# Performance work log

Measured on AMD Instinct MI355X. Metric: run time of the kernel, lower is better.

## Reference

```python
import jax, jax.numpy as jnp
import numpy as np

N, E, B = 30000, 60000, 500          # nodes, edges, graphs
NODE_IN, EDGE_IN, H, R = 64, 16, 64, 1024
MP_STEPS, S2S_STEPS = 3, 3           # num_step_message_passing, num_step_set2set
D = 2 * H                            # Set2Set in_channels / LSTM hidden size


def setup_inputs() -> dict:
    key = jax.random.key(0)
    ks = jax.random.split(key, 20)
    g = lambda i, shape, s: jax.random.normal(ks[i], shape, jnp.float32) * s
    return {
        "x": g(0, (N, NODE_IN), 1.0),
        "edge_index": jax.random.randint(ks[1], (2, E), 0, N),
        "edge_attr": g(2, (E, EDGE_IN), 1.0),
        "batch": jnp.sort(jax.random.randint(ks[3], (N,), 0, B)),
        # project_node_feats
        "W_proj": g(4, (NODE_IN, H), 0.1), "b_proj": jnp.zeros((H,), jnp.float32),
        # NNConv edge network + root + bias
        "W_edge": g(5, (EDGE_IN, H * H), 0.05), "b_edge": jnp.zeros((H * H,), jnp.float32),
        "root": g(6, (H, H), 0.1), "conv_bias": jnp.zeros((H,), jnp.float32),
        # GRU (torch gate order r, z, n)
        "gru_W_ih": g(7, (3 * H, H), 0.1), "gru_W_hh": g(8, (3 * H, H), 0.1),
        "gru_b_ih": jnp.zeros((3 * H,), jnp.float32), "gru_b_hh": jnp.zeros((3 * H,), jnp.float32),
        # node classifier head
        "W_cls": g(9, (H, 1), 0.1), "b_cls": jnp.zeros((1,), jnp.float32),
        # Set2Set LSTM: input 2D (=4H), hidden D (=2H), gate order i, f, g, o
        "lstm_W_ih": g(10, (4 * D, 2 * D), 0.1), "lstm_W_hh": g(11, (4 * D, D), 0.1),
        "lstm_b_ih": jnp.zeros((4 * D,), jnp.float32), "lstm_b_hh": jnp.zeros((4 * D,), jnp.float32),
        # sparsify (Linear 4H->R + PReLU)
        "W_sp": g(12, (4 * H, R), 0.05), "b_sp": jnp.zeros((R,), jnp.float32),
        "prelu_a": jnp.float32(0.25),
        "W_y1": g(13, (R, 128), 0.05), "b_y1": jnp.zeros((128,), jnp.float32),
        "W_y2": g(14, (128, 1), 0.1), "b_y2": jnp.zeros((1,), jnp.float32),
    }


def reference(x, edge_index, edge_attr, batch,
              W_proj, b_proj, W_edge, b_edge, root, conv_bias,
              gru_W_ih, gru_W_hh, gru_b_ih, gru_b_hh,
              W_cls, b_cls,
              lstm_W_ih, lstm_W_hh, lstm_b_ih, lstm_b_hh,
              W_sp, b_sp, prelu_a, W_y1, b_y1, W_y2, b_y2):
    src, dst = edge_index[0], edge_index[1]
    h0 = jax.nn.relu(x @ W_proj + b_proj)                  # [N, H]
    # Per-edge HxH weight matrices (loop-invariant; NNConv recomputes same values).
    We = (edge_attr @ W_edge + b_edge).reshape(E, H, H)    # [E, H, H]

    node, hidden = h0, h0
    for _ in range(MP_STEPS):
        msg = jnp.einsum('eh,eho->eo', node[src], We)      # gather + per-edge matvec
        aggr = jax.ops.segment_sum(msg, dst, num_segments=N)
        m = jax.nn.relu(aggr + node @ root + conv_bias)    # NNConv output + activation
        # GRU cell (seq_len=1)
        gi = m @ gru_W_ih.T + gru_b_ih
        gh = hidden @ gru_W_hh.T + gru_b_hh
        r = jax.nn.sigmoid(gi[:, :H] + gh[:, :H])
        z = jax.nn.sigmoid(gi[:, H:2 * H] + gh[:, H:2 * H])
        n = jnp.tanh(gi[:, 2 * H:] + r * gh[:, 2 * H:])
        hidden = (1.0 - z) * n + z * hidden
        node = hidden

    xcat = jnp.concatenate([h0, node], axis=1)             # [N, 2H] = [N, D]
    p_borylation = (node @ W_cls + b_cls)[:, 0]            # [N]

    # Set2Set over xcat
    q_star = jnp.zeros((B, 2 * D), xcat.dtype)
    hs = jnp.zeros((B, D), xcat.dtype)
    cs = jnp.zeros((B, D), xcat.dtype)
    for _ in range(S2S_STEPS):
        gts = q_star @ lstm_W_ih.T + lstm_b_ih + hs @ lstm_W_hh.T + lstm_b_hh
        i_g = jax.nn.sigmoid(gts[:, :D])
        f_g = jax.nn.sigmoid(gts[:, D:2 * D])
        g_g = jnp.tanh(gts[:, 2 * D:3 * D])
        o_g = jax.nn.sigmoid(gts[:, 3 * D:])
        cs = f_g * cs + i_g * g_g
        hs = o_g * jnp.tanh(cs)
        q = hs                                             # [B, D]
        e = jnp.sum(xcat * q[batch], axis=-1)              # [N]
        mseg = jax.ops.segment_max(e, batch, num_segments=B)
        ex = jnp.exp(e - mseg[batch])
        denom = jax.ops.segment_sum(ex, batch, num_segments=B)
        a = ex / denom[batch]                              # segment softmax
        rvec = jax.ops.segment_sum(a[:, None] * xcat, batch, num_segments=B)
        q_star = jnp.concatenate([q, rvec], axis=1)        # [B, 2D] = [B, 4H]

    gf = q_star @ W_sp + b_sp
    gf = jnp.where(gf >= 0, gf, prelu_a * gf)              # PReLU
    predicted_yield = (jax.nn.relu(gf @ W_y1 + b_y1) @ W_y2 + b_y2)[:, 0]
    return p_borylation, predicted_yield
```

## Files before the change

kernel.cpp:

```cpp
#include <hip/hip_runtime.h>
#include <math.h>

#define NN 30000
#define NNP 30080
#define NE 60000
#define NB 500
#define YGH 256
#define KE 1088

typedef __attribute__((ext_vector_type(8))) short bf16x8;
typedef __attribute__((ext_vector_type(4))) float f32x4;

__device__ __forceinline__ float sigmoidf_(float x) { return 1.0f / (1.0f + expf(-x)); }

__device__ __forceinline__ unsigned short bf_hi(float x) {
  unsigned int u = __float_as_uint(x);
  u += 0x7FFF + ((u >> 16) & 1);
  return (unsigned short)(u >> 16);
}
__device__ __forceinline__ float bf_f(unsigned short h) {
  return __uint_as_float(((unsigned int)h) << 16);
}
__device__ __forceinline__ void split_bf(float x, unsigned short& hi, unsigned short& lo) {
  hi = bf_hi(x);
  lo = bf_hi(x - bf_f(hi));
}

__device__ __forceinline__ int lower_bound_i(const int* __restrict__ a, int n, int v) {
  int lo = 0, hi = n;
  while (lo < hi) { int mid = (lo + hi) >> 1; if (a[mid] < v) lo = mid + 1; else hi = mid; }
  return lo;
}

__global__ __launch_bounds__(256) void gemm_mfma_k(
    const unsigned short* __restrict__ Ahi, const unsigned short* __restrict__ Alo,
    const unsigned short* __restrict__ Bhi, const unsigned short* __restrict__ Blo,
    float* __restrict__ C, int ldc,
    float* __restrict__ C2,
    unsigned short* __restrict__ Chi, unsigned short* __restrict__ Clo,
    const float* __restrict__ bias, int M, int flags)
{
  const int tid = threadIdx.x;
  const int wid = tid >> 6, lane = tid & 63;
  const int l15 = lane & 15, l4 = lane >> 4;
  const int r0 = blockIdx.x * 128 + (wid >> 1) * 64;
  const int c0 = blockIdx.y * 64 + (wid & 1) * 32;

  f32x4 acc[4][2];
#pragma unroll
  for (int rt = 0; rt < 4; rt++)
#pragma unroll
    for (int ct = 0; ct < 2; ct++) acc[rt][ct] = (f32x4){0.f, 0.f, 0.f, 0.f};

#pragma unroll
  for (int ks = 0; ks < 2; ks++) {
    const int kb = ks * 32 + l4 * 8;
    bf16x8 a_h[4], a_l[4], b_h[2], b_l[2];
#pragma unroll
    for (int rt = 0; rt < 4; rt++) {
      size_t off = (size_t)(r0 + rt * 16 + l15) * 64 + kb;
      a_h[rt] = *(const bf16x8*)(Ahi + off);
      a_l[rt] = *(const bf16x8*)(Alo + off);
    }
#pragma unroll
    for (int ct = 0; ct < 2; ct++) {
      size_t off = (size_t)(c0 + ct * 16 + l15) * 64 + kb;
      b_h[ct] = *(const bf16x8*)(Bhi + off);
      b_l[ct] = *(const bf16x8*)(Blo + off);
    }
#pragma unroll
    for (int rt = 0; rt < 4; rt++)
#pragma unroll
      for (int ct = 0; ct < 2; ct++) {
        acc[rt][ct] = __builtin_amdgcn_mfma_f32_16x16x32_bf16(a_h[rt], b_h[ct], acc[rt][ct], 0, 0, 0);
        acc[rt][ct] = __builtin_amdgcn_mfma_f32_16x16x32_bf16(a_h[rt], b_l[ct], acc[rt][ct], 0, 0, 0);
        acc[rt][ct] = __builtin_amdgcn_mfma_f32_16x16x32_bf16(a_l[rt], b_h[ct], acc[rt][ct], 0, 0, 0);
      }
  }

#pragma unroll
  for (int rt = 0; rt < 4; rt++) {
    const int rbase = r0 + rt * 16 + l4 * 4;
#pragma unroll
    for (int ct = 0; ct < 2; ct++) {
      const int col = c0 + ct * 16 + l15;
      const float bv = (flags & 1) ? bias[col] : 0.f;
#pragma unroll
      for (int reg = 0; reg < 4; reg++) {
        const int row = rbase + reg;
        if (row < M) {
          float v = acc[rt][ct][reg];
          if (flags & 1) v = fmaxf(v + bv, 0.f);
          C[(size_t)row * ldc + col] = v;
          if (flags & 4) C2[(size_t)row * 64 + col] = v;
          if (flags & 2) {
            unsigned short h, l;
            split_bf(v, h, l);
            Chi[(size_t)row * 64 + col] = h;
            Clo[(size_t)row * 64 + col] = l;
          }
        }
      }
    }
  }
}

__global__ __launch_bounds__(256) void edge_mfma_k(
    const int* __restrict__ ei, const float* __restrict__ ea,
    const float* __restrict__ h,
    const unsigned short* __restrict__ Whi, const unsigned short* __restrict__ Wlo,
    float* __restrict__ Yb)
{
  const int tid = threadIdx.x;
  const int wid = tid >> 6, lane = tid & 63;
  const int l15 = lane & 15, l4 = lane >> 4;
  const int e0 = (blockIdx.x * 4 + wid) * 64;

  int srcA[4];
  const float* eaA[4];
#pragma unroll
  for (int rt = 0; rt < 4; rt++) {
    int e = e0 + rt * 16 + l15;
    int ee = (e < NE) ? e : (NE - 1);
    srcA[rt] = ei[ee];
    eaA[rt] = ea + (size_t)ee * 16;
  }

  f32x4 acc[4][4];
#pragma unroll
  for (int rt = 0; rt < 4; rt++)
#pragma unroll
    for (int ct = 0; ct < 4; ct++) acc[rt][ct] = (f32x4){0.f, 0.f, 0.f, 0.f};

  for (int ks = 0; ks < KE / 32; ks++) {
    const int base = ks * 32 + l4 * 8;
    const int c = base >> 6;
    const int kb = base & 63;
    bf16x8 ah[4], al[4];
#pragma unroll
    for (int rt = 0; rt < 4; rt++) {
      float eac = (c < 16) ? eaA[rt][c] : 1.0f;
      const float* hp = h + (size_t)srcA[rt] * 64 + kb;
      float4 n0 = *(const float4*)hp;
      float4 n1 = *(const float4*)(hp + 4);
      float nv[8] = {n0.x, n0.y, n0.z, n0.w, n1.x, n1.y, n1.z, n1.w};
#pragma unroll
      for (int j = 0; j < 8; j++) {
        unsigned short hb, lb;
        split_bf(eac * nv[j], hb, lb);
        ah[rt][j] = (short)hb;
        al[rt][j] = (short)lb;
      }
    }
#pragma unroll
    for (int ct = 0; ct < 4; ct++) {
      size_t wo = (size_t)(ct * 16 + l15) * KE + base;
      bf16x8 bh = *(const bf16x8*)(Whi + wo);
      bf16x8 bl = *(const bf16x8*)(Wlo + wo);
#pragma unroll
      for (int rt = 0; rt < 4; rt++) {
        acc[rt][ct] = __builtin_amdgcn_mfma_f32_16x16x32_bf16(ah[rt], bh, acc[rt][ct], 0, 0, 0);
        acc[rt][ct] = __builtin_amdgcn_mfma_f32_16x16x32_bf16(ah[rt], bl, acc[rt][ct], 0, 0, 0);
        acc[rt][ct] = __builtin_amdgcn_mfma_f32_16x16x32_bf16(al[rt], bh, acc[rt][ct], 0, 0, 0);
      }
    }
  }

#pragma unroll
  for (int rt = 0; rt < 4; rt++) {
    const int er = e0 + rt * 16 + l4 * 4;
#pragma unroll
    for (int reg = 0; reg < 4; reg++) {
      const int e = er + reg;
      if (e < NE) {
        const int dst = ei[NE + e];
#pragma unroll
        for (int ct = 0; ct < 4; ct++)
          atomicAdd(&Yb[(size_t)dst * YGH + ct * 16 + l15], acc[rt][ct][reg]);
      }
    }
  }
}

__global__ __launch_bounds__(256) void prep_bt_k(
    const float* __restrict__ W_edge, const float* __restrict__ b_edge,
    const float* __restrict__ root, const float* __restrict__ gWhh,
    const float* __restrict__ gWih, const float* __restrict__ W_proj,
    unsigned short* __restrict__ BTbig_hi, unsigned short* __restrict__ BTbig_lo,
    unsigned short* __restrict__ W2_hi, unsigned short* __restrict__ W2_lo,
    unsigned short* __restrict__ BTih_hi, unsigned short* __restrict__ BTih_lo,
    unsigned short* __restrict__ BTp_hi, unsigned short* __restrict__ BTp_lo)
{
  int idx = blockIdx.x * 256 + threadIdx.x;
  const int NBIG = YGH * 64, NW2 = 64 * KE, NIH = 192 * 64, NP = 64 * 64;
  if (idx < NBIG) {
    int col = idx >> 6, k = idx & 63;
    float v = (col < 64) ? root[k * 64 + col] : gWhh[(size_t)(col - 64) * 64 + k];
    unsigned short h, l; split_bf(v, h, l);
    BTbig_hi[idx] = h; BTbig_lo[idx] = l;
  } else if (idx < NBIG + NW2) {
    int i2 = idx - NBIG;
    int o2 = i2 / KE, kq = i2 % KE;
    int c = kq >> 6, kk = kq & 63;
    float v = (c < 16) ? W_edge[(size_t)c * 4096 + kk * 64 + o2] : b_edge[kk * 64 + o2];
    unsigned short h, l; split_bf(v, h, l);
    W2_hi[i2] = h; W2_lo[i2] = l;
  } else if (idx < NBIG + NW2 + NIH) {
    int i2 = idx - NBIG - NW2;
    float v = gWih[i2];
    unsigned short h, l; split_bf(v, h, l);
    BTih_hi[i2] = h; BTih_lo[i2] = l;
  } else if (idx < NBIG + NW2 + NIH + NP) {
    int i2 = idx - NBIG - NW2 - NIH;
    int o2 = i2 >> 6, k = i2 & 63;
    float v = W_proj[k * 64 + o2];
    unsigned short h, l; split_bf(v, h, l);
    BTp_hi[i2] = h; BTp_lo[i2] = l;
  }
}

__global__ __launch_bounds__(256) void prep_lstmT_k(
    const float* __restrict__ Wih, const float* __restrict__ Whh,
    float* __restrict__ Tih, float* __restrict__ Thh)
{
  int idx = blockIdx.x * 256 + threadIdx.x;
  if (idx < 256 * 512) {
    int j = idx / 512, r = idx % 512;
    Tih[idx] = Wih[(size_t)r * 256 + j];
  } else if (idx < 256 * 512 + 128 * 512) {
    int id2 = idx - 256 * 512;
    int j = id2 / 512, r = id2 % 512;
    Thh[id2] = Whh[(size_t)r * 128 + j];
  }
}

__global__ __launch_bounds__(256) void split2_k(
    const float* __restrict__ src, unsigned short* __restrict__ hi,
    unsigned short* __restrict__ lo, int n4)
{
  int i = blockIdx.x * 256 + threadIdx.x;
  if (i >= n4) return;
  float4 v = ((const float4*)src)[i];
  unsigned short h0, l0, h1, l1, h2, l2, h3, l3;
  split_bf(v.x, h0, l0); split_bf(v.y, h1, l1);
  split_bf(v.z, h2, l2); split_bf(v.w, h3, l3);
  ((ushort4*)hi)[i] = make_ushort4(h0, h1, h2, h3);
  ((ushort4*)lo)[i] = make_ushort4(l0, l1, l2, l3);
}

__global__ __launch_bounds__(256) void m_relu_split_k(
    const float* __restrict__ Yb, const float* __restrict__ conv_b,
    unsigned short* __restrict__ mbh, unsigned short* __restrict__ mbl)
{
  int t = blockIdx.x * 256 + threadIdx.x;
  if (t >= NN * 64) return;
  int n = t >> 6, c = t & 63;
  float v = fmaxf(Yb[(size_t)n * YGH + c] + conv_b[c], 0.f);
  unsigned short h, l; split_bf(v, h, l);
  mbh[t] = h; mbl[t] = l;
}

__global__ __launch_bounds__(256) void gru_split_k(
    const float* __restrict__ gi, const float* __restrict__ Yb,
    const float* __restrict__ bih, const float* __restrict__ bhh,
    float* __restrict__ h, unsigned short* __restrict__ hh, unsigned short* __restrict__ hl)
{
  int t = blockIdx.x * 256 + threadIdx.x;
  if (t >= NN * 64) return;
  int n = t >> 6, c = t & 63;
  const float* gin = gi + (size_t)n * 192;
  const float* ghn = Yb + (size_t)n * YGH + 64;
  float r = sigmoidf_(gin[c] + bih[c] + ghn[c] + bhh[c]);
  float z = sigmoidf_(gin[64 + c] + bih[64 + c] + ghn[64 + c] + bhh[64 + c]);
  float ng = tanhf(gin[128 + c] + bih[128 + c] + r * (ghn[128 + c] + bhh[128 + c]));
  float hv = h[t];
  float hn = (1.f - z) * ng + z * hv;
  h[t] = hn;
  unsigned short hb, lb; split_bf(hn, hb, lb);
  hh[t] = hb; hl[t] = lb;
}

__global__ __launch_bounds__(256) void cls_xcat_k(
    const float* __restrict__ h, const float* __restrict__ Wcls,
    const float* __restrict__ bcls, float* __restrict__ xcat, float* __restrict__ out)
{
  int gw = (blockIdx.x * blockDim.x + threadIdx.x) >> 6;
  if (gw >= NN) return;
  int lane = threadIdx.x & 63;
  float hv = h[(size_t)gw * 64 + lane];
  xcat[(size_t)gw * 128 + 64 + lane] = hv;
  float p = hv * Wcls[lane];
#pragma unroll
  for (int off = 32; off > 0; off >>= 1) p += __shfl_xor(p, off);
  if (lane == 0) out[gw] = p + bcls[0];
}

__global__ __launch_bounds__(256) void gemmK_k(
    const float* __restrict__ A, int lda,
    const float* __restrict__ B, int ldb,
    float* __restrict__ C, int ldc,
    const float* __restrict__ Csrc,
    const float* __restrict__ bias, const float* __restrict__ alpha_p,
    int M, int K, int flags)
{
  __shared__ float As[64 * 68];
  __shared__ float Bs[64 * 64];
  const int tid = threadIdx.x;
  const int m0 = blockIdx.x * 64;
  const int n0 = blockIdx.y * 64;
  const int tx = tid & 15, ty = tid >> 4;
  float acc[4][4] = {};

  for (int kc = 0; kc < K; kc += 64) {
#pragma unroll
    for (int i = 0; i < 4; i++) {
      int f4 = tid + i * 256;
      int row = f4 >> 4;
      int kk = (f4 & 15) << 2;
      float4 v = make_float4(0.f, 0.f, 0.f, 0.f);
      if (m0 + row < M) v = *(const float4*)(A + (size_t)(m0 + row) * lda + kc + kk);
      *(float4*)&As[row * 68 + kk] = v;
    }
#pragma unroll
    for (int i = 0; i < 4; i++) {
      int f4 = tid + i * 256;
      int kk = f4 >> 4;
      int nn = (f4 & 15) << 2;
      float4 v = *(const float4*)(B + (size_t)(kc + kk) * ldb + n0 + nn);
      *(float4*)&Bs[kk * 64 + nn] = v;
    }
    __syncthreads();
    const float* As0 = As + (ty * 4 + 0) * 68;
    const float* As1 = As + (ty * 4 + 1) * 68;
    const float* As2 = As + (ty * 4 + 2) * 68;
    const float* As3 = As + (ty * 4 + 3) * 68;
#pragma unroll
    for (int k = 0; k < 64; k++) {
      float4 b = *(const float4*)(Bs + k * 64 + tx * 4);
      float a0 = As0[k], a1 = As1[k], a2 = As2[k], a3 = As3[k];
      acc[0][0] = fmaf(a0, b.x, acc[0][0]); acc[0][1] = fmaf(a0, b.y, acc[0][1]);
      acc[0][2] = fmaf(a0, b.z, acc[0][2]); acc[0][3] = fmaf(a0, b.w, acc[0][3]);
      acc[1][0] = fmaf(a1, b.x, acc[1][0]); acc[1][1] = fmaf(a1, b.y, acc[1][1]);
      acc[1][2] = fmaf(a1, b.z, acc[1][2]); acc[1][3] = fmaf(a1, b.w, acc[1][3]);
      acc[2][0] = fmaf(a2, b.x, acc[2][0]); acc[2][1] = fmaf(a2, b.y, acc[2][1]);
      acc[2][2] = fmaf(a2, b.z, acc[2][2]); acc[2][3] = fmaf(a2, b.w, acc[2][3]);
      acc[3][0] = fmaf(a3, b.x, acc[3][0]); acc[3][1] = fmaf(a3, b.y, acc[3][1]);
      acc[3][2] = fmaf(a3, b.z, acc[3][2]); acc[3][3] = fmaf(a3, b.w, acc[3][3]);
    }
    __syncthreads();
  }

  const int coln = tx * 4;
  const int col = n0 + coln;
  float alpha = (flags & 32) ? alpha_p[0] : 0.f;
#pragma unroll
  for (int i = 0; i < 4; i++) {
    int row = m0 + ty * 4 + i;
    if (row < M) {
      float v0 = acc[i][0], v1 = acc[i][1], v2 = acc[i][2], v3 = acc[i][3];
      size_t off = (size_t)row * ldc + col;
      if (flags & 4) {
        float4 s = *(const float4*)(Csrc + off);
        v0 += s.x; v1 += s.y; v2 += s.z; v3 += s.w;
      }
      if (flags & 1) {
        v0 += bias[col + 0]; v1 += bias[col + 1]; v2 += bias[col + 2]; v3 += bias[col + 3];
      }
      if (flags & 2) {
        v0 = fmaxf(v0, 0.f); v1 = fmaxf(v1, 0.f); v2 = fmaxf(v2, 0.f); v3 = fmaxf(v3, 0.f);
      }
      if (flags & 32) {
        v0 = (v0 >= 0.f) ? v0 : alpha * v0; v1 = (v1 >= 0.f) ? v1 : alpha * v1;
        v2 = (v2 >= 0.f) ? v2 : alpha * v2; v3 = (v3 >= 0.f) ? v3 : alpha * v3;
      }
      *(float4*)&C[off] = make_float4(v0, v1, v2, v3);
    }
  }
}

__global__ __launch_bounds__(256) void lstm_elem_k(
    const float* __restrict__ gts, const float* __restrict__ bih, const float* __restrict__ bhh,
    float* __restrict__ hs, float* __restrict__ cs)
{
  int t = blockIdx.x * 256 + threadIdx.x;
  if (t >= NB * 128) return;
  int b = t >> 7, d = t & 127;
  const float* g = gts + (size_t)b * 512;
  float iv = sigmoidf_(g[d] + bih[d] + bhh[d]);
  float fv = sigmoidf_(g[128 + d] + bih[128 + d] + bhh[128 + d]);
  float gv = tanhf(g[256 + d] + bih[256 + d] + bhh[256 + d]);
  float ov = sigmoidf_(g[384 + d] + bih[384 + d] + bhh[384 + d]);
  float c = fv * cs[t] + iv * gv;
  cs[t] = c;
  hs[t] = ov * tanhf(c);
}

__global__ __launch_bounds__(256) void attn_k(
    const float* __restrict__ xcat, const int* __restrict__ batch,
    const float* __restrict__ hs, float* __restrict__ e_ws, float* __restrict__ q_star)
{
  __shared__ float q[128];
  __shared__ float red[4];
  __shared__ float rvw[4 * 128];
  __shared__ float dw[4];
  __shared__ int se[2];
  int b = blockIdx.x;
  int tid = threadIdx.x;
  if (tid < 128) q[tid] = hs[(size_t)b * 128 + tid];
  if (tid == 254) se[0] = lower_bound_i(batch, NN, b);
  if (tid == 255) se[1] = lower_bound_i(batch, NN, b + 1);
  __syncthreads();
  int start = se[0], end = se[1];
  int lane = tid & 63, w = tid >> 6;
  float wmax = -INFINITY;
  for (int n = start + w; n < end; n += 4) {
    const float* xr = xcat + (size_t)n * 128;
    float p = xr[lane] * q[lane] + xr[64 + lane] * q[64 + lane];
#pragma unroll
    for (int off = 32; off > 0; off >>= 1) p += __shfl_xor(p, off);
    if (lane == 0) e_ws[n] = p;
    wmax = fmaxf(wmax, p);
  }
  if (lane == 0) red[w] = wmax;
  __syncthreads();
  float bmax = fmaxf(fmaxf(red[0], red[1]), fmaxf(red[2], red[3]));
  float a0 = 0.f, a1 = 0.f, ds = 0.f;
  for (int n = start + w; n < end; n += 4) {
    float ex = expf(e_ws[n] - bmax);
    const float* xr = xcat + (size_t)n * 128;
    a0 = fmaf(ex, xr[lane], a0);
    a1 = fmaf(ex, xr[64 + lane], a1);
    ds += ex;
  }
  rvw[w * 128 + lane] = a0;
  rvw[w * 128 + 64 + lane] = a1;
  if (lane == 0) dw[w] = ds;
  __syncthreads();
  if (tid < 128) {
    float r = rvw[tid] + rvw[128 + tid] + rvw[256 + tid] + rvw[384 + tid];
    float dsum = dw[0] + dw[1] + dw[2] + dw[3];
    q_star[(size_t)b * 256 + tid] = q[tid];
    q_star[(size_t)b * 256 + 128 + tid] = (end > start) ? (r / dsum) : 0.f;
  }
}

__global__ __launch_bounds__(256) void yout_k(
    const float* __restrict__ y1, const float* __restrict__ Wy2,
    const float* __restrict__ by2, float* __restrict__ out)
{
  int gw = (blockIdx.x * blockDim.x + threadIdx.x) >> 6;
  if (gw >= NB) return;
  int lane = threadIdx.x & 63;
  const float* yr = y1 + (size_t)gw * 128;
  float p = yr[lane] * Wy2[lane] + yr[64 + lane] * Wy2[64 + lane];
#pragma unroll
  for (int off = 32; off > 0; off >>= 1) p += __shfl_xor(p, off);
  if (lane == 0) out[gw] = p + by2[0];
}

extern "C" void kernel_launch(void* const* d_in, const int* in_sizes, int n_in,
                              void* d_out, int out_size, void* d_ws, size_t ws_size,
                              hipStream_t stream) {
  const float* x      = (const float*)d_in[0];
  const int*   ei     = (const int*)d_in[1];
  const float* ea     = (const float*)d_in[2];
  const int*   batch  = (const int*)d_in[3];
  const float* W_proj = (const float*)d_in[4];
  const float* b_proj = (const float*)d_in[5];
  const float* W_edge = (const float*)d_in[6];
  const float* b_edge = (const float*)d_in[7];
  const float* root   = (const float*)d_in[8];
  const float* conv_b = (const float*)d_in[9];
  const float* gWih   = (const float*)d_in[10];
  const float* gWhh   = (const float*)d_in[11];
  const float* gbih   = (const float*)d_in[12];
  const float* gbhh   = (const float*)d_in[13];
  const float* Wcls   = (const float*)d_in[14];
  const float* bcls   = (const float*)d_in[15];
  const float* lWih   = (const float*)d_in[16];
  const float* lWhh   = (const float*)d_in[17];
  const float* lbih   = (const float*)d_in[18];
  const float* lbhh   = (const float*)d_in[19];
  const float* Wsp    = (const float*)d_in[20];
  const float* bsp    = (const float*)d_in[21];
  const float* pa     = (const float*)d_in[22];
  const float* Wy1    = (const float*)d_in[23];
  const float* by1    = (const float*)d_in[24];
  const float* Wy2    = (const float*)d_in[25];
  const float* by2    = (const float*)d_in[26];
  float* out = (float*)d_out;

  float* ws = (float*)d_ws;
  size_t o = 0;
  float* h      = ws + o; o += (size_t)NN * 64;
  float* Ybig   = ws + o; o += (size_t)NN * YGH;
  float* gi     = ws + o; o += (size_t)NN * 192;
  float* xcat   = ws + o; o += (size_t)NN * 128;
  float* e_ws   = ws + o; o += (size_t)NN;
  float* q_star = ws + o; o += (size_t)NB * 256;
  float* hs     = ws + o; o += (size_t)NB * 128;
  float* cs     = ws + o; o += (size_t)NB * 128;
  float* Tih    = ws + o; o += 256 * 512;
  float* Thh    = ws + o; o += 128 * 512;
  float* gts    = ws + o; o += (size_t)NB * 512;
  float* gf     = ws + o; o += (size_t)NB * 1024;
  float* y1     = ws + o; o += (size_t)NB * 128;

  unsigned short* us = (unsigned short*)(ws + o);
  size_t u = 0;
  unsigned short* hh_b   = us + u; u += (size_t)NNP * 64;
  unsigned short* hl_b   = us + u; u += (size_t)NNP * 64;
  unsigned short* mbh    = us + u; u += (size_t)NNP * 64;
  unsigned short* mbl    = us + u; u += (size_t)NNP * 64;
  unsigned short* BTb_hi = us + u; u += (size_t)YGH * 64;
  unsigned short* BTb_lo = us + u; u += (size_t)YGH * 64;
  unsigned short* W2_hi  = us + u; u += (size_t)64 * KE;
  unsigned short* W2_lo  = us + u; u += (size_t)64 * KE;
  unsigned short* BTi_hi = us + u; u += (size_t)192 * 64;
  unsigned short* BTi_lo = us + u; u += (size_t)192 * 64;
  unsigned short* BTp_hi = us + u; u += (size_t)64 * 64;
  unsigned short* BTp_lo = us + u; u += (size_t)64 * 64;

  const int MT = NNP / 128;
  const int ET = (NE + 255) / 256;
  const int PREP_N = YGH * 64 + 64 * KE + 192 * 64 + 64 * 64;

  prep_bt_k<<<(PREP_N + 255) / 256, 256, 0, stream>>>(
      W_edge, b_edge, root, gWhh, gWih, W_proj,
      BTb_hi, BTb_lo, W2_hi, W2_lo, BTi_hi, BTi_lo, BTp_hi, BTp_lo);
  prep_lstmT_k<<<768, 256, 0, stream>>>(lWih, lWhh, Tih, Thh);
  split2_k<<<(NN * 16 + 255) / 256, 256, 0, stream>>>(x, hh_b, hl_b, NN * 16);

  gemm_mfma_k<<<dim3(MT, 1), 256, 0, stream>>>(hh_b, hl_b, BTp_hi, BTp_lo,
                                               xcat, 128, h, hh_b, hl_b, b_proj, NN, 1 | 2 | 4);
  for (int step = 0; step < 3; step++) {
    gemm_mfma_k<<<dim3(MT, YGH / 64), 256, 0, stream>>>(hh_b, hl_b, BTb_hi, BTb_lo,
                                                        Ybig, YGH, nullptr, nullptr, nullptr,
                                                        nullptr, NN, 0);
    edge_mfma_k<<<ET, 256, 0, stream>>>(ei, ea, h, W2_hi, W2_lo, Ybig);
    m_relu_split_k<<<(NN * 64) / 256, 256, 0, stream>>>(Ybig, conv_b, mbh, mbl);
    gemm_mfma_k<<<dim3(MT, 3), 256, 0, stream>>>(mbh, mbl, BTi_hi, BTi_lo,
                                                 gi, 192, nullptr, nullptr, nullptr,
                                                 nullptr, NN, 0);
    gru_split_k<<<(NN * 64) / 256, 256, 0, stream>>>(gi, Ybig, gbih, gbhh, h, hh_b, hl_b);
  }
  cls_xcat_k<<<(NN * 64) / 256, 256, 0, stream>>>(h, Wcls, bcls, xcat, out);
  hipMemsetAsync(q_star, 0, (size_t)NB * (256 + 128 + 128) * sizeof(float), stream);
  for (int t = 0; t < 3; t++) {
    gemmK_k<<<dim3(8, 8), 256, 0, stream>>>(q_star, 256, Tih, 512, gts, 512,
                                            nullptr, nullptr, nullptr, NB, 256, 0);
    gemmK_k<<<dim3(8, 8), 256, 0, stream>>>(hs, 128, Thh, 512, gts, 512,
                                            gts, nullptr, nullptr, NB, 128, 4);
    lstm_elem_k<<<(NB * 128 + 255) / 256, 256, 0, stream>>>(gts, lbih, lbhh, hs, cs);
    attn_k<<<NB, 256, 0, stream>>>(xcat, batch, hs, e_ws, q_star);
  }
  gemmK_k<<<dim3(8, 16), 256, 0, stream>>>(q_star, 256, Wsp, 1024, gf, 1024,
                                           nullptr, bsp, pa, NB, 256, 1 | 32);
  gemmK_k<<<dim3(8, 2), 256, 0, stream>>>(gf, 1024, Wy1, 128, y1, 128,
                                          nullptr, by1, nullptr, NB, 1024, 1 | 2);
  yout_k<<<(NB * 64 + 255) / 256, 256, 0, stream>>>(y1, Wy2, by2, out + NN);
}
```

Measured before the change: 776.2 us.

## Restructure edge MFMA per 16 edges, fold LSTM hh into ih, fuse LSTM into attention

```diff
diff --git a/kernel.cpp b/kernel.cpp
--- a/kernel.cpp
+++ b/kernel.cpp
@@ -108,76 +108,80 @@
 __global__ __launch_bounds__(256) void edge_mfma_k(
     const int* __restrict__ ei, const float* __restrict__ ea,
     const float* __restrict__ h,
+    const unsigned short* __restrict__ hh, const unsigned short* __restrict__ hl,
     const unsigned short* __restrict__ Whi, const unsigned short* __restrict__ Wlo,
     float* __restrict__ Yb)
 {
   const int tid = threadIdx.x;
   const int wid = tid >> 6, lane = tid & 63;
   const int l15 = lane & 15, l4 = lane >> 4;
-  const int e0 = (blockIdx.x * 4 + wid) * 64;
-
-  int srcA[4];
-  const float* eaA[4];
-#pragma unroll
-  for (int rt = 0; rt < 4; rt++) {
-    int e = e0 + rt * 16 + l15;
-    int ee = (e < NE) ? e : (NE - 1);
-    srcA[rt] = ei[ee];
-    eaA[rt] = ea + (size_t)ee * 16;
-  }
-
-  f32x4 acc[4][4];
-#pragma unroll
-  for (int rt = 0; rt < 4; rt++)
-#pragma unroll
-    for (int ct = 0; ct < 4; ct++) acc[rt][ct] = (f32x4){0.f, 0.f, 0.f, 0.f};
-
-  for (int ks = 0; ks < KE / 32; ks++) {
-    const int base = ks * 32 + l4 * 8;
-    const int c = base >> 6;
-    const int kb = base & 63;
-    bf16x8 ah[4], al[4];
-#pragma unroll
-    for (int rt = 0; rt < 4; rt++) {
-      float eac = (c < 16) ? eaA[rt][c] : 1.0f;
-      const float* hp = h + (size_t)srcA[rt] * 64 + kb;
-      float4 n0 = *(const float4*)hp;
-      float4 n1 = *(const float4*)(hp + 4);
-      float nv[8] = {n0.x, n0.y, n0.z, n0.w, n1.x, n1.y, n1.z, n1.w};
-#pragma unroll
-      for (int j = 0; j < 8; j++) {
-        unsigned short hb, lb;
-        split_bf(eac * nv[j], hb, lb);
-        ah[rt][j] = (short)hb;
-        al[rt][j] = (short)lb;
-      }
-    }
-#pragma unroll
-    for (int ct = 0; ct < 4; ct++) {
-      size_t wo = (size_t)(ct * 16 + l15) * KE + base;
-      bf16x8 bh = *(const bf16x8*)(Whi + wo);
-      bf16x8 bl = *(const bf16x8*)(Wlo + wo);
-#pragma unroll
-      for (int rt = 0; rt < 4; rt++) {
-        acc[rt][ct] = __builtin_amdgcn_mfma_f32_16x16x32_bf16(ah[rt], bh, acc[rt][ct], 0, 0, 0);
-        acc[rt][ct] = __builtin_amdgcn_mfma_f32_16x16x32_bf16(ah[rt], bl, acc[rt][ct], 0, 0, 0);
-        acc[rt][ct] = __builtin_amdgcn_mfma_f32_16x16x32_bf16(al[rt], bh, acc[rt][ct], 0, 0, 0);
-      }
-    }
-  }
-
-#pragma unroll
-  for (int rt = 0; rt < 4; rt++) {
-    const int er = e0 + rt * 16 + l4 * 4;
-#pragma unroll
-    for (int reg = 0; reg < 4; reg++) {
-      const int e = er + reg;
-      if (e < NE) {
-        const int dst = ei[NE + e];
-#pragma unroll
-        for (int ct = 0; ct < 4; ct++)
-          atomicAdd(&Yb[(size_t)dst * YGH + ct * 16 + l15], acc[rt][ct][reg]);
-      }
+  const int e0 = (blockIdx.x * 4 + wid) * 16;
+  if (e0 >= NE) return;
+  const int kb = l4 * 8;
+
+  const int e = e0 + l15;
+  const int ee = (e < NE) ? e : (NE - 1);
+  const int src = ei[ee];
+
+  const float* eap = ea + (size_t)ee * 16;
+  float4 ea0 = *(const float4*)(eap + 0);
+  float4 ea1 = *(const float4*)(eap + 4);
+  float4 ea2 = *(const float4*)(eap + 8);
+  float4 ea3 = *(const float4*)(eap + 12);
+  float eav[16] = {ea0.x, ea0.y, ea0.z, ea0.w, ea1.x, ea1.y, ea1.z, ea1.w,
+                   ea2.x, ea2.y, ea2.z, ea2.w, ea3.x, ea3.y, ea3.z, ea3.w};
+  const float* hp = h + (size_t)src * 64 + kb;
+  float4 hv0 = *(const float4*)(hp);
+  float4 hv1 = *(const float4*)(hp + 4);
+  float4 hv2 = *(const float4*)(hp + 32);
+  float4 hv3 = *(const float4*)(hp + 36);
+
+  f32x4 acc[4];
+#pragma unroll
+  for (int ct = 0; ct < 4; ct++) acc[ct] = (f32x4){0.f, 0.f, 0.f, 0.f};
+
+  for (int c = 0; c < 17; c++) {
+#pragma unroll
+    for (int ks = 0; ks < 2; ks++) {
+      bf16x8 ah, al;
+      if (c < 16) {
+        const float eac = eav[c];
+        const float4 va = ks ? hv2 : hv0;
+        const float4 vb = ks ? hv3 : hv1;
+        const float nv[8] = {va.x, va.y, va.z, va.w, vb.x, vb.y, vb.z, vb.w};
+#pragma unroll
+        for (int j = 0; j < 8; j++) {
+          unsigned short hb, lb;
+          split_bf(eac * nv[j], hb, lb);
+          ah[j] = (short)hb;
+          al[j] = (short)lb;
+        }
+      } else {
+        size_t off = (size_t)src * 64 + ks * 32 + kb;
+        ah = *(const bf16x8*)(hh + off);
+        al = *(const bf16x8*)(hl + off);
+      }
+      const int base = c * 64 + ks * 32 + kb;
+#pragma unroll
+      for (int ct = 0; ct < 4; ct++) {
+        size_t wo = (size_t)(ct * 16 + l15) * KE + base;
+        bf16x8 bh = *(const bf16x8*)(Whi + wo);
+        bf16x8 bl = *(const bf16x8*)(Wlo + wo);
+        acc[ct] = __builtin_amdgcn_mfma_f32_16x16x32_bf16(ah, bh, acc[ct], 0, 0, 0);
+        acc[ct] = __builtin_amdgcn_mfma_f32_16x16x32_bf16(ah, bl, acc[ct], 0, 0, 0);
+        acc[ct] = __builtin_amdgcn_mfma_f32_16x16x32_bf16(al, bh, acc[ct], 0, 0, 0);
+      }
+    }
+  }
+
+#pragma unroll
+  for (int reg = 0; reg < 4; reg++) {
+    const int es = e0 + l4 * 4 + reg;
+    if (es < NE) {
+      const int dst = ei[NE + es];
+#pragma unroll
+      for (int ct = 0; ct < 4; ct++)
+        atomicAdd(&Yb[(size_t)dst * YGH + ct * 16 + l15], acc[ct][reg]);
     }
   }
 }
@@ -219,19 +223,15 @@
   }
 }
 
-__global__ __launch_bounds__(256) void prep_lstmT_k(
-    const float* __restrict__ Wih, const float* __restrict__ Whh,
-    float* __restrict__ Tih, float* __restrict__ Thh)
+__global__ __launch_bounds__(256) void prep_tcomb_k(
+    const float* __restrict__ Wih, const float* __restrict__ Whh, float* __restrict__ T)
 {
   int idx = blockIdx.x * 256 + threadIdx.x;
-  if (idx < 256 * 512) {
-    int j = idx / 512, r = idx % 512;
-    Tih[idx] = Wih[(size_t)r * 256 + j];
-  } else if (idx < 256 * 512 + 128 * 512) {
-    int id2 = idx - 256 * 512;
-    int j = id2 / 512, r = id2 % 512;
-    Thh[id2] = Whh[(size_t)r * 128 + j];
-  }
+  if (idx >= 256 * 512) return;
+  int j = idx / 512, r = idx % 512;
+  float v = Wih[(size_t)r * 256 + j];
+  if (j < 128) v += Whh[(size_t)r * 128 + j];
+  T[idx] = v;
 }
 
 __global__ __launch_bounds__(256) void split2_k(
@@ -378,26 +378,11 @@
   }
 }
 
-__global__ __launch_bounds__(256) void lstm_elem_k(
+__global__ __launch_bounds__(256) void lstm_attn_k(
     const float* __restrict__ gts, const float* __restrict__ bih, const float* __restrict__ bhh,
-    float* __restrict__ hs, float* __restrict__ cs)
-{
-  int t = blockIdx.x * 256 + threadIdx.x;
-  if (t >= NB * 128) return;
-  int b = t >> 7, d = t & 127;
-  const float* g = gts + (size_t)b * 512;
-  float iv = sigmoidf_(g[d] + bih[d] + bhh[d]);
-  float fv = sigmoidf_(g[128 + d] + bih[128 + d] + bhh[128 + d]);
-  float gv = tanhf(g[256 + d] + bih[256 + d] + bhh[256 + d]);
-  float ov = sigmoidf_(g[384 + d] + bih[384 + d] + bhh[384 + d]);
-  float c = fv * cs[t] + iv * gv;
-  cs[t] = c;
-  hs[t] = ov * tanhf(c);
-}
-
-__global__ __launch_bounds__(256) void attn_k(
+    float* __restrict__ cs,
     const float* __restrict__ xcat, const int* __restrict__ batch,
-    const float* __restrict__ hs, float* __restrict__ e_ws, float* __restrict__ q_star)
+    float* __restrict__ e_ws, float* __restrict__ q_star)
 {
   __shared__ float q[128];
   __shared__ float red[4];
@@ -406,7 +391,17 @@
   __shared__ int se[2];
   int b = blockIdx.x;
   int tid = threadIdx.x;
-  if (tid < 128) q[tid] = hs[(size_t)b * 128 + tid];
+  if (tid < 128) {
+    int d = tid;
+    const float* g = gts + (size_t)b * 512;
+    float iv = sigmoidf_(g[d] + bih[d] + bhh[d]);
+    float fv = sigmoidf_(g[128 + d] + bih[128 + d] + bhh[128 + d]);
+    float gv = tanhf(g[256 + d] + bih[256 + d] + bhh[256 + d]);
+    float ov = sigmoidf_(g[384 + d] + bih[384 + d] + bhh[384 + d]);
+    float c = fv * cs[(size_t)b * 128 + d] + iv * gv;
+    cs[(size_t)b * 128 + d] = c;
+    q[d] = ov * tanhf(c);
+  }
   if (tid == 254) se[0] = lower_bound_i(batch, NN, b);
   if (tid == 255) se[1] = lower_bound_i(batch, NN, b + 1);
   __syncthreads();
@@ -498,10 +493,8 @@
   float* xcat   = ws + o; o += (size_t)NN * 128;
   float* e_ws   = ws + o; o += (size_t)NN;
   float* q_star = ws + o; o += (size_t)NB * 256;
-  float* hs     = ws + o; o += (size_t)NB * 128;
   float* cs     = ws + o; o += (size_t)NB * 128;
-  float* Tih    = ws + o; o += 256 * 512;
-  float* Thh    = ws + o; o += 128 * 512;
+  float* Tcomb  = ws + o; o += 256 * 512;
   float* gts    = ws + o; o += (size_t)NB * 512;
   float* gf     = ws + o; o += (size_t)NB * 1024;
   float* y1     = ws + o; o += (size_t)NB * 128;
@@ -522,13 +515,13 @@
   unsigned short* BTp_lo = us + u; u += (size_t)64 * 64;
 
   const int MT = NNP / 128;
-  const int ET = (NE + 255) / 256;
+  const int ET = (NE + 63) / 64;
   const int PREP_N = YGH * 64 + 64 * KE + 192 * 64 + 64 * 64;
 
   prep_bt_k<<<(PREP_N + 255) / 256, 256, 0, stream>>>(
       W_edge, b_edge, root, gWhh, gWih, W_proj,
       BTb_hi, BTb_lo, W2_hi, W2_lo, BTi_hi, BTi_lo, BTp_hi, BTp_lo);
-  prep_lstmT_k<<<768, 256, 0, stream>>>(lWih, lWhh, Tih, Thh);
+  prep_tcomb_k<<<512, 256, 0, stream>>>(lWih, lWhh, Tcomb);
   split2_k<<<(NN * 16 + 255) / 256, 256, 0, stream>>>(x, hh_b, hl_b, NN * 16);
 
   gemm_mfma_k<<<dim3(MT, 1), 256, 0, stream>>>(hh_b, hl_b, BTp_hi, BTp_lo,
@@ -537,7 +530,7 @@
     gemm_mfma_k<<<dim3(MT, YGH / 64), 256, 0, stream>>>(hh_b, hl_b, BTb_hi, BTb_lo,
                                                         Ybig, YGH, nullptr, nullptr, nullptr,
                                                         nullptr, NN, 0);
-    edge_mfma_k<<<ET, 256, 0, stream>>>(ei, ea, h, W2_hi, W2_lo, Ybig);
+    edge_mfma_k<<<ET, 256, 0, stream>>>(ei, ea, h, hh_b, hl_b, W2_hi, W2_lo, Ybig);
     m_relu_split_k<<<(NN * 64) / 256, 256, 0, stream>>>(Ybig, conv_b, mbh, mbl);
     gemm_mfma_k<<<dim3(MT, 3), 256, 0, stream>>>(mbh, mbl, BTi_hi, BTi_lo,
                                                  gi, 192, nullptr, nullptr, nullptr,
@@ -545,14 +538,11 @@
     gru_split_k<<<(NN * 64) / 256, 256, 0, stream>>>(gi, Ybig, gbih, gbhh, h, hh_b, hl_b);
   }
   cls_xcat_k<<<(NN * 64) / 256, 256, 0, stream>>>(h, Wcls, bcls, xcat, out);
-  hipMemsetAsync(q_star, 0, (size_t)NB * (256 + 128 + 128) * sizeof(float), stream);
+  hipMemsetAsync(q_star, 0, (size_t)NB * (256 + 128) * sizeof(float), stream);
   for (int t = 0; t < 3; t++) {
-    gemmK_k<<<dim3(8, 8), 256, 0, stream>>>(q_star, 256, Tih, 512, gts, 512,
+    gemmK_k<<<dim3(8, 8), 256, 0, stream>>>(q_star, 256, Tcomb, 512, gts, 512,
                                             nullptr, nullptr, nullptr, NB, 256, 0);
-    gemmK_k<<<dim3(8, 8), 256, 0, stream>>>(hs, 128, Thh, 512, gts, 512,
-                                            gts, nullptr, nullptr, NB, 128, 4);
-    lstm_elem_k<<<(NB * 128 + 255) / 256, 256, 0, stream>>>(gts, lbih, lbhh, hs, cs);
-    attn_k<<<NB, 256, 0, stream>>>(xcat, batch, hs, e_ws, q_star);
+    lstm_attn_k<<<NB, 256, 0, stream>>>(gts, lbih, lbhh, cs, xcat, batch, e_ws, q_star);
   }
   gemmK_k<<<dim3(8, 16), 256, 0, stream>>>(q_star, 256, Wsp, 1024, gf, 1024,
                                            nullptr, bsp, pa, NB, 256, 1 | 32);
```

Measured after the change: 847.0 us. 9.1% more time.
